# Performance work log

Hardware: AMD Instinct MI355X
Metric: run time of the kernel (lower is better)

The kernel has to match this reference:

```python
import jax, jax.numpy as jnp
import numpy as np

jax.config.update("jax_enable_x64", True)

TOL = 1e-06


def setup_inputs() -> dict:
    key = jax.random.key(0)
    k1, k2 = jax.random.split(key)
    n, d = 4096, 128
    output = jax.random.normal(k1, (n, d), dtype=jnp.float32)
    # target: square roots of patristic distances -> nonnegative
    target = jax.random.uniform(k2, (n, n), dtype=jnp.float32) * 2.0
    return {"output": output, "target": target}


def reference(output, target):
    # Torch module casts to double before all math
    out = output.astype(jnp.float64)
    tgt = target.astype(jnp.float64)
    n = out.shape[0]

    # Lorentz inner product: B = outer(s, s) - out @ out.T, s = sqrt(1 + ||o||^2)
    s = jnp.sqrt(1.0 + jnp.sum(out * out, axis=1))          # [n]
    B = s[:, None] * s[None, :] - out @ out.T               # [n, n]

    # Clamp near-1 entries exactly to 1 (torch: B[(B-1).abs() < tol] = 1.0)
    clamp = jnp.abs(B - 1.0) < TOL
    # Safe acosh: evaluate at 2.0 where clamped to avoid inf/nan, then set dist=0 there
    B_safe = jnp.where(clamp, 2.0, B)
    dist = jnp.where(clamp, 0.0, jnp.arccosh(B_safe))       # acosh(1) == 0

    # Strictly-lower-triangular masked MAE
    tril_mask = jnp.tril(jnp.ones((n, n), dtype=jnp.float64), k=-1)
    loss = jnp.sum(jnp.abs(dist - tgt) * tril_mask) / (n * (n - 1))
    return loss
```

## Files before the change

### kernel.cpp

```cpp
#include <hip/hip_runtime.h>
#include <math.h>

#define N 4096
#define D 128
#define TS 64
#define NT (N / TS)
#define NBLK (NT * (NT + 1) / 2)
#define NG (N / 16)
#define TPAD 68

typedef __attribute__((ext_vector_type(8))) short short8;
typedef __attribute__((ext_vector_type(4))) float f32x4;

union frag_u { short8 v; unsigned int u[4]; };

__device__ __forceinline__ unsigned int pack_bf16x2(float a, float b) {
    unsigned int ua = __float_as_uint(a), ub = __float_as_uint(b);
    ua = (ua + 0x7FFFu + ((ua >> 16) & 1u)) >> 16;
    ub = (ub + 0x7FFFu + ((ub >> 16) & 1u)) >> 16;
    return ua | (ub << 16);
}

__global__ __launch_bounds__(256)
void prep_kernel(const float* __restrict__ O,
                 short8* __restrict__ Ofrag,
                 float* __restrict__ s) {
    __shared__ float psum[16][17];
    const int g    = blockIdx.x;
    const int tid  = threadIdx.x;
    const int kk   = tid >> 6;
    const int lane = tid & 63;
    const int r16  = lane & 15;
    const int qd   = lane >> 4;
    const float* src = O + (size_t)(g * 16 + r16) * D + kk * 32 + qd * 8;
    const float4 v0 = *(const float4*)(src);
    const float4 v1 = *(const float4*)(src + 4);
    frag_u f;
    f.u[0] = pack_bf16x2(v0.x, v0.y);
    f.u[1] = pack_bf16x2(v0.z, v0.w);
    f.u[2] = pack_bf16x2(v1.x, v1.y);
    f.u[3] = pack_bf16x2(v1.z, v1.w);
    Ofrag[(g * 4 + kk) * 64 + lane] = f.v;
    psum[kk * 4 + qd][r16] = v0.x * v0.x + v0.y * v0.y + v0.z * v0.z + v0.w * v0.w
                           + v1.x * v1.x + v1.y * v1.y + v1.z * v1.z + v1.w * v1.w;
    __syncthreads();
    if (tid < 16) {
        float acc = 1.0f;
        #pragma unroll
        for (int x = 0; x < 16; x++) acc += psum[x][tid];
        s[g * 16 + tid] = sqrtf(acc);
    }
}

__device__ __forceinline__ float acosh_dist(float B) {
    if (fabsf(B - 1.0f) < 1e-6f) return 0.0f;
    const float Bc = fmaxf(B, 1.0f);
    return __log2f(Bc + sqrtf(fmaf(Bc, Bc, -1.0f))) * 0.6931471805599453f;
}

__global__ __launch_bounds__(256, 8)
void tile_loss_kernel(const short8* __restrict__ Fr,
                      const float* __restrict__ s,
                      const float* __restrict__ tgt,
                      float* __restrict__ partials) {
    __shared__ float T[TS][TPAD];
    __shared__ float wsum[4];

    const int t = blockIdx.x;
    int ti = (int)((sqrtf(8.0f * (float)t + 1.0f) - 1.0f) * 0.5f);
    while ((ti + 1) * (ti + 2) / 2 <= t) ti++;
    while (ti * (ti + 1) / 2 > t) ti--;
    const int tj = t - ti * (ti + 1) / 2;

    const int tid  = threadIdx.x;
    const int wave = tid >> 6;
    const int lane = tid & 63;
    const int quad = lane >> 4;
    const int l16  = lane & 15;

    const int ib0 = ti * TS;
    const int jb  = tj * TS;
    const int r0  = wave * 16 + quad * 4;

    const int rr = tid >> 4;
    const int cc = (tid & 15) * 4;
    float4 tg[4];
    #pragma unroll
    for (int p = 0; p < 4; p++)
        tg[p] = *(const float4*)(tgt + (size_t)(ib0 + p * 16 + rr) * N + jb + cc);

    float sj[4];
    #pragma unroll
    for (int n = 0; n < 4; n++) sj[n] = s[jb + n * 16 + l16];
    float si[4];
    #pragma unroll
    for (int r = 0; r < 4; r++) si[r] = s[ib0 + r0 + r];

    f32x4 acc[4] = {};
    const int ga4 = (ti * 4 + wave) * 4;
    const int gb4 = tj * 4 * 4;
    #pragma unroll
    for (int kp = 0; kp < 2; kp++) {
        const int k0 = kp * 2, k1 = kp * 2 + 1;
        const short8 a0 = Fr[(ga4 + k0) * 64 + lane];
        const short8 a1 = Fr[(ga4 + k1) * 64 + lane];
        short8 b0[4], b1[4];
        #pragma unroll
        for (int n = 0; n < 4; n++) {
            b0[n] = Fr[(gb4 + n * 4 + k0) * 64 + lane];
            b1[n] = Fr[(gb4 + n * 4 + k1) * 64 + lane];
        }
        #pragma unroll
        for (int n = 0; n < 4; n++)
            acc[n] = __builtin_amdgcn_mfma_f32_16x16x32_bf16(a0, b0[n], acc[n], 0, 0, 0);
        #pragma unroll
        for (int n = 0; n < 4; n++)
            acc[n] = __builtin_amdgcn_mfma_f32_16x16x32_bf16(a1, b1[n], acc[n], 0, 0, 0);
    }

    #pragma unroll
    for (int p = 0; p < 4; p++)
        *(float4*)&T[p * 16 + rr][cc] = tg[p];
    __syncthreads();

    float lsum = 0.0f;
    if (ti != tj) {
        #pragma unroll
        for (int r = 0; r < 4; r++)
            #pragma unroll
            for (int n = 0; n < 4; n++) {
                const float B  = fmaf(si[r], sj[n], -acc[n][r]);
                const float tv = T[r0 + r][n * 16 + l16];
                lsum += fabsf(acosh_dist(B) - tv);
            }
    } else {
        #pragma unroll
        for (int r = 0; r < 4; r++) {
            const int i = ib0 + r0 + r;
            #pragma unroll
            for (int n = 0; n < 4; n++) {
                const int j = jb + n * 16 + l16;
                if (j < i) {
                    const float B  = fmaf(si[r], sj[n], -acc[n][r]);
                    const float tv = T[r0 + r][n * 16 + l16];
                    lsum += fabsf(acosh_dist(B) - tv);
                }
            }
        }
    }

    #pragma unroll
    for (int off = 32; off > 0; off >>= 1)
        lsum += __shfl_down(lsum, off, 64);
    if (lane == 0) wsum[wave] = lsum;
    __syncthreads();
    if (tid == 0)
        partials[t] = wsum[0] + wsum[1] + wsum[2] + wsum[3];
}

__global__ __launch_bounds__(256)
void final_reduce_kernel(const float* __restrict__ partials,
                         float* __restrict__ loss) {
    __shared__ float wsum[4];
    const int tid  = threadIdx.x;
    const int wave = tid >> 6;
    const int lane = tid & 63;
    float acc = 0.0f;
    for (int i = tid; i < NBLK; i += 256) acc += partials[i];
    #pragma unroll
    for (int off = 32; off > 0; off >>= 1)
        acc += __shfl_down(acc, off, 64);
    if (lane == 0) wsum[wave] = acc;
    __syncthreads();
    if (tid == 0) {
        const float tot = wsum[0] + wsum[1] + wsum[2] + wsum[3];
        loss[0] = tot * (1.0f / ((float)N * (float)(N - 1)));
    }
}

extern "C" void kernel_launch(void* const* d_in, const int* in_sizes, int n_in,
                              void* d_out, int out_size, void* d_ws, size_t ws_size,
                              hipStream_t stream) {
    const float* O   = (const float*)d_in[0];
    const float* tgt = (const float*)d_in[1];
    float* loss = (float*)d_out;

    short8* Ofrag = (short8*)d_ws;
    float* s        = (float*)((char*)d_ws + (size_t)N * D * 2);
    float* partials = s + N;

    prep_kernel<<<NG, 256, 0, stream>>>(O, Ofrag, s);
    tile_loss_kernel<<<NBLK, 256, 0, stream>>>(Ofrag, s, tgt, partials);
    final_reduce_kernel<<<1, 256, 0, stream>>>(partials, loss);
}
```

Baseline: 119.5 us.

## Stream target tile directly to LDS via global_load_lds and preload all MFMA fragments

```diff
diff --git a/kernel.cpp b/kernel.cpp
--- a/kernel.cpp
+++ b/kernel.cpp
@@ -7,7 +7,6 @@
 #define NT (N / TS)
 #define NBLK (NT * (NT + 1) / 2)
 #define NG (N / 16)
-#define TPAD 68
 
 typedef __attribute__((ext_vector_type(8))) short short8;
 typedef __attribute__((ext_vector_type(4))) float f32x4;
@@ -58,12 +57,19 @@
     return __log2f(Bc + sqrtf(fmaf(Bc, Bc, -1.0f))) * 0.6931471805599453f;
 }
 
-__global__ __launch_bounds__(256, 8)
+__device__ __forceinline__ void gload_lds16(const float* g, float* l) {
+    __builtin_amdgcn_global_load_lds(
+        (const __attribute__((address_space(1))) unsigned int*)g,
+        (__attribute__((address_space(3))) unsigned int*)l,
+        16, 0, 0);
+}
+
+__global__ __launch_bounds__(256, 4)
 void tile_loss_kernel(const short8* __restrict__ Fr,
                       const float* __restrict__ s,
                       const float* __restrict__ tgt,
                       float* __restrict__ partials) {
-    __shared__ float T[TS][TPAD];
+    __shared__ float T[TS][TS];
     __shared__ float wsum[4];
 
     const int t = blockIdx.x;
@@ -82,12 +88,15 @@
     const int jb  = tj * TS;
     const int r0  = wave * 16 + quad * 4;
 
-    const int rr = tid >> 4;
-    const int cc = (tid & 15) * 4;
-    float4 tg[4];
+    const int ga4 = (ti * 4 + wave) * 4;
+    const int gb4 = tj * 4 * 4;
+    short8 a[4], b[4][4];
     #pragma unroll
-    for (int p = 0; p < 4; p++)
-        tg[p] = *(const float4*)(tgt + (size_t)(ib0 + p * 16 + rr) * N + jb + cc);
+    for (int k = 0; k < 4; k++) a[k] = Fr[(ga4 + k) * 64 + lane];
+    #pragma unroll
+    for (int n = 0; n < 4; n++)
+        #pragma unroll
+        for (int k = 0; k < 4; k++) b[n][k] = Fr[(gb4 + n * 4 + k) * 64 + lane];
 
     float sj[4];
     #pragma unroll
@@ -96,31 +105,22 @@
     #pragma unroll
     for (int r = 0; r < 4; r++) si[r] = s[ib0 + r0 + r];
 
+    {
+        const float* gsrc = tgt + (size_t)(ib0 + wave * 16 + (lane >> 4)) * N
+                          + jb + (lane & 15) * 4;
+        #pragma unroll
+        for (int q = 0; q < 4; q++)
+            gload_lds16(gsrc + (size_t)q * 4 * N, &T[wave * 16 + q * 4][0]);
+    }
+
     f32x4 acc[4] = {};
-    const int ga4 = (ti * 4 + wave) * 4;
-    const int gb4 = tj * 4 * 4;
     #pragma unroll
-    for (int kp = 0; kp < 2; kp++) {
-        const int k0 = kp * 2, k1 = kp * 2 + 1;
-        const short8 a0 = Fr[(ga4 + k0) * 64 + lane];
-        const short8 a1 = Fr[(ga4 + k1) * 64 + lane];
-        short8 b0[4], b1[4];
-        #pragma unroll
-        for (int n = 0; n < 4; n++) {
-            b0[n] = Fr[(gb4 + n * 4 + k0) * 64 + lane];
-            b1[n] = Fr[(gb4 + n * 4 + k1) * 64 + lane];
-        }
+    for (int k = 0; k < 4; k++)
         #pragma unroll
         for (int n = 0; n < 4; n++)
-            acc[n] = __builtin_amdgcn_mfma_f32_16x16x32_bf16(a0, b0[n], acc[n], 0, 0, 0);
-        #pragma unroll
-        for (int n = 0; n < 4; n++)
-            acc[n] = __builtin_amdgcn_mfma_f32_16x16x32_bf16(a1, b1[n], acc[n], 0, 0, 0);
-    }
+            acc[n] = __builtin_amdgcn_mfma_f32_16x16x32_bf16(a[k], b[n][k], acc[n], 0, 0, 0);
 
-    #pragma unroll
-    for (int p = 0; p < 4; p++)
-        *(float4*)&T[p * 16 + rr][cc] = tg[p];
+    asm volatile("s_waitcnt vmcnt(0)" ::: "memory");
     __syncthreads();
 
     float lsum = 0.0f;
```

Measured after the change: 103.3 us. -13.5%, faster.
